# Kernel tuning notes

Hardware: AMD Instinct MI355X
Metric: run time of the kernel (lower is better)

## Reference

```python
import jax, jax.numpy as jnp
import numpy as np

N_HEADS = 4


def grid_sample_bilinear(img, grid):
    # img: (B, C, H, W); grid: (B, *S, 2) with (x, y) in [-1, 1]; torch bilinear, align_corners=True
    B, C, H, W = img.shape
    sp = grid.shape[1:-1]
    g = grid.reshape(B, -1, 2)
    x = (g[..., 0] + 1.0) * 0.5 * (W - 1)
    y = (g[..., 1] + 1.0) * 0.5 * (H - 1)
    x0 = jnp.floor(x)
    y0 = jnp.floor(y)
    wx = x - x0
    wy = y - y0
    x0i = jnp.clip(x0, 0, W - 1).astype(jnp.int32)
    x1i = jnp.clip(x0 + 1, 0, W - 1).astype(jnp.int32)
    y0i = jnp.clip(y0, 0, H - 1).astype(jnp.int32)
    y1i = jnp.clip(y0 + 1, 0, H - 1).astype(jnp.int32)
    flat = img.reshape(B, C, H * W)
    take = jax.vmap(lambda f, i: f[:, i])  # (C, HW), (N,) -> (C, N)
    out = (take(flat, y0i * W + x0i) * ((1 - wx) * (1 - wy))[:, None, :]
           + take(flat, y0i * W + x1i) * (wx * (1 - wy))[:, None, :]
           + take(flat, y1i * W + x0i) * ((1 - wx) * wy)[:, None, :]
           + take(flat, y1i * W + x1i) * (wx * wy)[:, None, :])
    return out.reshape((B, C) + sp)


def dw_conv_k4s4(x, w, b):
    # depthwise conv, kernel=4, stride=4, pad=0 (kernel == stride): non-overlapping patches
    B, C, H, W = x.shape
    xr = x.reshape(B, C, H // 4, 4, W // 4, 4)
    return jnp.einsum('bchpwq,cpq->bchw', xr, w) + b[None, :, None, None]


def ln_channels(x, g, b, eps=1e-5):
    # LayerNormProxy: LayerNorm over channel dim of NCHW
    mu = jnp.mean(x, axis=1, keepdims=True)
    var = jnp.var(x, axis=1, keepdims=True)
    return (x - mu) * jax.lax.rsqrt(var + eps) * g[None, :, None, None] + b[None, :, None, None]


def ref_points(Hk, Wk):
    ry = jnp.linspace(0.5, Hk - 0.5, Hk) / (Hk - 1.0) * 2.0 - 1.0
    rx = jnp.linspace(0.5, Wk - 0.5, Wk) / (Wk - 1.0) * 2.0 - 1.0
    return jnp.stack(jnp.meshgrid(ry, rx, indexing='ij'), axis=-1)  # (Hk, Wk, 2) as (y, x)


def q_grid(H, W):
    ry = jnp.arange(H, dtype=jnp.float32) / (H - 1.0) * 2.0 - 1.0
    rx = jnp.arange(W, dtype=jnp.float32) / (W - 1.0) * 2.0 - 1.0
    return jnp.stack(jnp.meshgrid(ry, rx, indexing='ij'), axis=-1).reshape(H * W, 2)


def dat_block(x, p):
    # DAttentionBaseline: n_groups=1, stride=ksize=4, offset_range_factor=-1, use_pe (learned rpe table)
    dw_w, dw_b, ln_g, ln_b, pw_w, wq, bq, wk, bk, wv, bv, wo, bo, rpe = p
    B, C, H, W = x.shape
    hc = C // N_HEADS
    scale = hc ** -0.5
    q = jnp.einsum('oc,bchw->bohw', wq, x) + bq[None, :, None, None]
    t = jax.nn.gelu(ln_channels(dw_conv_k4s4(q, dw_w, dw_b), ln_g, ln_b), approximate=False)
    off = jnp.einsum('oc,bchw->bohw', pw_w, t)  # (B, 2, Hk, Wk), channels = (dy, dx)
    Hk, Wk = off.shape[2], off.shape[3]
    ns = Hk * Wk
    pos = jnp.clip(off.transpose(0, 2, 3, 1) + ref_points(Hk, Wk)[None], -1.0, 1.0)  # (B,Hk,Wk,2) (y,x)
    xs = grid_sample_bilinear(x, pos[..., ::-1]).reshape(B, C, ns)  # kv == q input here
    k = jnp.einsum('oc,bcn->bon', wk, xs) + bk[None, :, None]
    v = jnp.einsum('oc,bcn->bon', wv, xs) + bv[None, :, None]
    qh = q.reshape(B, N_HEADS, hc, H * W)
    attn = jnp.einsum('bhcm,bhcn->bhmn', qh, k.reshape(B, N_HEADS, hc, ns)) * scale
    disp = (q_grid(H, W)[None, :, None, :] - pos.reshape(B, 1, ns, 2)) * 0.5  # (B, HW, ns, 2) (y,x)
    rpe_b = jnp.broadcast_to(rpe[None], (B,) + rpe.shape)
    attn = attn + grid_sample_bilinear(rpe_b, disp[..., ::-1])  # (B, heads, HW, ns)
    attn = jax.nn.softmax(attn, axis=-1)
    out = jnp.einsum('bhmn,bhcn->bhcm', attn, v.reshape(B, N_HEADS, hc, ns)).reshape(B, C, H, W)
    return jnp.einsum('oc,bchw->bohw', wo, out) + bo[None, :, None, None]


def _block_params(key, c, H, W):
    ks = jax.random.split(key, 7)
    return dict(
        off_dw_w=0.05 * jax.random.normal(ks[0], (c, 4, 4), dtype=jnp.float32),
        off_dw_b=jnp.zeros((c,), jnp.float32),
        ln_g=jnp.ones((c,), jnp.float32),
        ln_b=jnp.zeros((c,), jnp.float32),
        off_pw_w=0.02 * jax.random.normal(ks[1], (2, c), dtype=jnp.float32),
        wq=0.02 * jax.random.normal(ks[2], (c, c), dtype=jnp.float32),
        bq=jnp.zeros((c,), jnp.float32),
        wk=0.02 * jax.random.normal(ks[3], (c, c), dtype=jnp.float32),
        bk=jnp.zeros((c,), jnp.float32),
        wv=0.02 * jax.random.normal(ks[4], (c, c), dtype=jnp.float32),
        bv=jnp.zeros((c,), jnp.float32),
        wo=0.02 * jax.random.normal(ks[5], (c, c), dtype=jnp.float32),
        bo=jnp.zeros((c,), jnp.float32),
        rpe=0.01 * jax.random.normal(ks[6], (N_HEADS, 2 * H - 1, 2 * W - 1), dtype=jnp.float32),
    )


def setup_inputs() -> dict:
    key = jax.random.key(0)
    k0, k1, k2 = jax.random.split(key, 3)
    B, C, H, W = 8, 512, 64, 64
    inp = {'x0': jax.random.normal(k0, (B, C, H, W), dtype=jnp.float32)}
    for pre, k in (('sc_', k1), ('tr_', k2)):
        for n, v in _block_params(k, C // 2, H, W).items():
            inp[pre + n] = v
    return inp


def reference(x0,
              sc_off_dw_w, sc_off_dw_b, sc_ln_g, sc_ln_b, sc_off_pw_w, sc_wq, sc_bq, sc_wk, sc_bk,
              sc_wv, sc_bv, sc_wo, sc_bo, sc_rpe,
              tr_off_dw_w, tr_off_dw_b, tr_ln_g, tr_ln_b, tr_off_pw_w, tr_wq, tr_bq, tr_wk, tr_bk,
              tr_wv, tr_bv, tr_wo, tr_bo, tr_rpe):
    B, C, H, W = x0.shape
    qc1 = C // 2
    q = x0[:, :qc1]
    sc_p = (sc_off_dw_w, sc_off_dw_b, sc_ln_g, sc_ln_b, sc_off_pw_w, sc_wq, sc_bq, sc_wk, sc_bk,
            sc_wv, sc_bv, sc_wo, sc_bo, sc_rpe)
    tr_p = (tr_off_dw_w, tr_off_dw_b, tr_ln_g, tr_ln_b, tr_off_pw_w, tr_wq, tr_bq, tr_wk, tr_bk,
            tr_wv, tr_bv, tr_wo, tr_bo, tr_rpe)
    s = dat_block(q, sc_p)
    t = dat_block(q, tr_p)
    z = jnp.zeros((B, C - qc1, H, W), x0.dtype)
    scale_full = jnp.concatenate([z, s], axis=1)
    trans_full = jnp.concatenate([z, t], axis=1)
    res = x0 * jnp.exp(scale_full) + trans_full
    jac = jnp.sum(scale_full, axis=(1, 2, 3))[None, :]  # (n_vars=1, B)
    return res, jac
```

## Files before the change

kernel.cpp:

```cpp
#include <hip/hip_runtime.h>
#include <math.h>

typedef __bf16 bf16;
typedef __attribute__((ext_vector_type(8))) __bf16 bf16x8;
typedef __attribute__((ext_vector_type(4))) __bf16 bf16x4;
typedef __attribute__((ext_vector_type(4))) float floatx4;

#define MFMA16(a, b, c) __builtin_amdgcn_mfma_f32_16x16x32_bf16((a), (b), (c), 0, 0, 0)

__device__ __forceinline__ float bflo(unsigned d) {
    unsigned u = d << 16; float f; __builtin_memcpy(&f, &u, 4); return f;
}
__device__ __forceinline__ float bfhi(unsigned d) {
    unsigned u = d & 0xffff0000u; float f; __builtin_memcpy(&f, &u, 4); return f;
}

__device__ __forceinline__ void breduce1(float &a, float* lds, int t) {
    #pragma unroll
    for (int off = 32; off; off >>= 1) a += __shfl_xor(a, off, 64);
    __syncthreads();
    if ((t & 63) == 0) lds[t >> 6] = a;
    __syncthreads();
    a = lds[0] + lds[1] + lds[2] + lds[3];
}

__global__ __launch_bounds__(256) void init_kernel(const float* __restrict__ x0,
                                                   float* __restrict__ out) {
    int fi = blockIdx.x * 256 + threadIdx.x;
    int b = fi >> 18;
    int r = fi & 262143;
    const float4* src = (const float4*)x0;
    float4* dst = (float4*)out;
    dst[(size_t)b * 524288 + r] = src[(size_t)b * 524288 + r];
}

__global__ __launch_bounds__(256) void wconv(
    const float* __restrict__ w0, const float* __restrict__ w1,
    const float* __restrict__ w2, const float* __restrict__ w3,
    const float* __restrict__ w4, const float* __restrict__ w5,
    const float* __restrict__ w6, const float* __restrict__ w7,
    bf16* __restrict__ dst) {
    const int wi = blockIdx.y;
    const float* src = wi == 0 ? w0 : wi == 1 ? w1 : wi == 2 ? w2 : wi == 3 ? w3
                     : wi == 4 ? w4 : wi == 5 ? w5 : wi == 6 ? w6 : w7;
    const int i = blockIdx.x * 1024 + threadIdx.x * 4;
    const float4 v = *(const float4*)(src + i);
    bf16x4 h, l;
    #pragma unroll
    for (int j = 0; j < 4; j++) {
        const float f = ((const float*)&v)[j];
        const bf16 hb = (bf16)f;
        h[j] = hb;
        l[j] = (bf16)(f - (float)hb);
    }
    *(bf16x4*)(dst + (size_t)wi * 65536 + i) = h;
    *(bf16x4*)(dst + (size_t)(8 + wi) * 65536 + i) = l;
}

template <int MODE>
__global__ __launch_bounds__(256) void gemm_mfma(
    const void* __restrict__ Aptr, int ldA, long long bsA,
    const bf16* __restrict__ Whi, const bf16* __restrict__ Wlo,
    const float* __restrict__ bias,
    bf16* __restrict__ outb,
    float* outf,
    const float* __restrict__ x0full,
    float* __restrict__ jpart)
{
    constexpr bool ASPLIT = (MODE <= 2);
    __shared__ __align__(16) bf16 As_hi[128 * 40];
    __shared__ __align__(16) bf16 As_lo[ASPLIT ? 128 * 40 : 1];
    __shared__ __align__(16) bf16 Bs_hi[128 * 40];
    __shared__ __align__(16) bf16 Bs_lo[128 * 40];
    __shared__ float red[4];
    const int t = threadIdx.x;
    const int b = blockIdx.z;
    const int n0 = blockIdx.x * 128;
    const int o0 = blockIdx.y * 128;
    const int w = t >> 6, l = t & 63;
    const int wr = w & 1, wc = w >> 1;
    const int lr = l & 15, lq = l >> 4;

    floatx4 acc[4][4] = {};

    for (int kb = 0; kb < 8; kb++) {
        if (ASPLIT) {
            const float* Af = (const float*)Aptr + (size_t)b * bsA;
            #pragma unroll
            for (int s = 0; s < 4; s++) {
                const int kk = s * 8 + (t >> 5);
                const int n = (t & 31) * 4;
                const float4 v = *(const float4*)(Af + (size_t)(kb * 32 + kk) * ldA + n0 + n);
                #pragma unroll
                for (int j = 0; j < 4; j++) {
                    const float f = ((const float*)&v)[j];
                    const bf16 hb = (bf16)f;
                    As_hi[(n + j) * 40 + kk] = hb;
                    As_lo[(n + j) * 40 + kk] = (bf16)(f - (float)hb);
                }
            }
        } else {
            const bf16* Ab = (const bf16*)Aptr + (size_t)b * bsA;
            #pragma unroll
            for (int s = 0; s < 2; s++) {
                const int idx = t + 256 * s;
                const int row = idx >> 2, seg = idx & 3;
                *(bf16x8*)(As_hi + row * 40 + seg * 8) =
                    *(const bf16x8*)(Ab + (size_t)(n0 + row) * 256 + kb * 32 + seg * 8);
            }
        }
        #pragma unroll
        for (int s = 0; s < 2; s++) {
            const int idx = t + 256 * s;
            const int row = idx >> 2, seg = idx & 3;
            *(bf16x8*)(Bs_hi + row * 40 + seg * 8) =
                *(const bf16x8*)(Whi + (size_t)(o0 + row) * 256 + kb * 32 + seg * 8);
            *(bf16x8*)(Bs_lo + row * 40 + seg * 8) =
                *(const bf16x8*)(Wlo + (size_t)(o0 + row) * 256 + kb * 32 + seg * 8);
        }
        __syncthreads();
        bf16x8 ah[4], al[4], bh[4], bl[4];
        #pragma unroll
        for (int f = 0; f < 4; f++) {
            ah[f] = *(const bf16x8*)(As_hi + (wr * 64 + f * 16 + lr) * 40 + lq * 8);
            if (ASPLIT)
                al[f] = *(const bf16x8*)(As_lo + (wr * 64 + f * 16 + lr) * 40 + lq * 8);
            bh[f] = *(const bf16x8*)(Bs_hi + (wc * 64 + f * 16 + lr) * 40 + lq * 8);
            bl[f] = *(const bf16x8*)(Bs_lo + (wc * 64 + f * 16 + lr) * 40 + lq * 8);
        }
        #pragma unroll
        for (int i = 0; i < 4; i++)
            #pragma unroll
            for (int j = 0; j < 4; j++) {
                acc[i][j] = MFMA16(ah[i], bh[j], acc[i][j]);
                acc[i][j] = MFMA16(ah[i], bl[j], acc[i][j]);
                if (ASPLIT) acc[i][j] = MFMA16(al[i], bh[j], acc[i][j]);
            }
        __syncthreads();
    }

    float ssum = 0.0f;
    #pragma unroll
    for (int i = 0; i < 4; i++) {
        #pragma unroll
        for (int j = 0; j < 4; j++) {
            const int o_g = o0 + wc * 64 + j * 16 + lr;
            const int n_b = n0 + wr * 64 + i * 16 + lq * 4;
            const float bia = bias[o_g];
            floatx4 val = acc[i][j];
            val[0] += bia; val[1] += bia; val[2] += bia; val[3] += bia;
            if (MODE == 0) {
                *(floatx4*)(outf + (size_t)b * 2097152 + (size_t)o_g * 4096 + n_b) = val;
                #pragma unroll
                for (int r = 0; r < 4; r++)
                    outb[((size_t)b * 4096 + n_b + r) * 256 + o_g] = (bf16)val[r];
            } else {
                const size_t addr = (size_t)b * 2097152 + (size_t)(256 + o_g) * 4096 + n_b;
                if (MODE == 3) {
                    *(floatx4*)(outf + addr) = val;
                } else {
                    const floatx4 s4 = *(const floatx4*)(outf + addr);
                    const floatx4 x4 = *(const floatx4*)(x0full + addr);
                    floatx4 res;
                    #pragma unroll
                    for (int r = 0; r < 4; r++) res[r] = x4[r] * expf(s4[r]) + val[r];
                    *(floatx4*)(outf + addr) = res;
                    ssum += s4[0] + s4[1] + s4[2] + s4[3];
                }
            }
        }
    }
    if (MODE == 4) {
        breduce1(ssum, red, t);
        if (t == 0) jpart[b * 64 + blockIdx.y * 32 + blockIdx.x] = ssum;
    }
}

__global__ __launch_bounds__(256) void gemm_kv(
    const bf16* __restrict__ xs_hi, const bf16* __restrict__ xs_lo,
    const bf16* __restrict__ wkh, const bf16* __restrict__ wkl,
    const bf16* __restrict__ wvh, const bf16* __restrict__ wvl,
    const float* __restrict__ bk, const float* __restrict__ bv,
    bf16* __restrict__ kT, bf16* __restrict__ vbuf)
{
    __shared__ __align__(16) bf16 As_hi[128 * 40];
    __shared__ __align__(16) bf16 As_lo[128 * 40];
    __shared__ __align__(16) bf16 Bs_hi[128 * 40];
    __shared__ __align__(16) bf16 Bs_lo[128 * 40];
    const int t = threadIdx.x;
    const int b = blockIdx.z;
    const int n0 = blockIdx.x * 128;
    const int kv = blockIdx.y >> 1;
    const int o0 = (blockIdx.y & 1) * 128;
    const bf16* Whi = kv ? wvh : wkh;
    const bf16* Wlo = kv ? wvl : wkl;
    const float* bias = kv ? bv : bk;
    const int w = t >> 6, l = t & 63;
    const int wr = w & 1, wc = w >> 1;
    const int lr = l & 15, lq = l >> 4;

    floatx4 acc[4][4] = {};

    for (int kb = 0; kb < 8; kb++) {
        #pragma unroll
        for (int s = 0; s < 2; s++) {
            const int idx = t + 256 * s;
            const int row = idx >> 2, seg = idx & 3;
            const size_t asrc = ((size_t)b * 256 + n0 + row) * 256 + kb * 32 + seg * 8;
            *(bf16x8*)(As_hi + row * 40 + seg * 8) = *(const bf16x8*)(xs_hi + asrc);
            *(bf16x8*)(As_lo + row * 40 + seg * 8) = *(const bf16x8*)(xs_lo + asrc);
            *(bf16x8*)(Bs_hi + row * 40 + seg * 8) =
                *(const bf16x8*)(Whi + (size_t)(o0 + row) * 256 + kb * 32 + seg * 8);
            *(bf16x8*)(Bs_lo + row * 40 + seg * 8) =
                *(const bf16x8*)(Wlo + (size_t)(o0 + row) * 256 + kb * 32 + seg * 8);
        }
        __syncthreads();
        bf16x8 ah[4], al[4], bh[4], bl[4];
        #pragma unroll
        for (int f = 0; f < 4; f++) {
            ah[f] = *(const bf16x8*)(As_hi + (wr * 64 + f * 16 + lr) * 40 + lq * 8);
            al[f] = *(const bf16x8*)(As_lo + (wr * 64 + f * 16 + lr) * 40 + lq * 8);
            bh[f] = *(const bf16x8*)(Bs_hi + (wc * 64 + f * 16 + lr) * 40 + lq * 8);
            bl[f] = *(const bf16x8*)(Bs_lo + (wc * 64 + f * 16 + lr) * 40 + lq * 8);
        }
        #pragma unroll
        for (int i = 0; i < 4; i++)
            #pragma unroll
            for (int j = 0; j < 4; j++) {
                acc[i][j] = MFMA16(ah[i], bh[j], acc[i][j]);
                acc[i][j] = MFMA16(ah[i], bl[j], acc[i][j]);
                acc[i][j] = MFMA16(al[i], bh[j], acc[i][j]);
            }
        __syncthreads();
    }

    #pragma unroll
    for (int i = 0; i < 4; i++) {
        #pragma unroll
        for (int j = 0; j < 4; j++) {
            const int o_g = o0 + wc * 64 + j * 16 + lr;
            const int n_b = n0 + wr * 64 + i * 16 + lq * 4;
            const float bia = bias[o_g];
            floatx4 val = acc[i][j];
            val[0] += bia; val[1] += bia; val[2] += bia; val[3] += bia;
            if (kv == 0) {
                #pragma unroll
                for (int r = 0; r < 4; r++)
                    kT[((size_t)b * 256 + n_b + r) * 256 + o_g] = (bf16)val[r];
            } else {
                bf16x4 pv;
                pv[0] = (bf16)val[0]; pv[1] = (bf16)val[1];
                pv[2] = (bf16)val[2]; pv[3] = (bf16)val[3];
                *(bf16x4*)(vbuf + ((size_t)b * 256 + o_g) * 256 + n_b) = pv;
            }
        }
    }
}

__global__ __launch_bounds__(64) void jac_reduce(const float* __restrict__ jpart,
                                                 float* __restrict__ out) {
    const int b = blockIdx.x, t = threadIdx.x;
    float v = jpart[b * 64 + t];
    #pragma unroll
    for (int off = 32; off; off >>= 1) v += __shfl_xor(v, off, 64);
    if (t == 0) out[16777216 + b] = v;
}

__global__ __launch_bounds__(256) void offset_kernel(
    const float* __restrict__ q,
    const float* __restrict__ dw_w, const float* __restrict__ dw_b,
    const float* __restrict__ ln_g, const float* __restrict__ ln_b,
    const float* __restrict__ pw_w,
    float* __restrict__ pos)
{
    __shared__ float red[8];
    const int wk = blockIdx.x, hk = blockIdx.y, b = blockIdx.z;
    const int c = threadIdx.x;
    const float* qp = q + (size_t)b * 2097152 + (size_t)c * 4096 + (hk * 4) * 64 + wk * 4;
    float accv = dw_b[c];
    #pragma unroll
    for (int p = 0; p < 4; p++) {
        const float4 r = *(const float4*)(qp + p * 64);
        const float4 w = *(const float4*)(dw_w + c * 16 + p * 4);
        accv += r.x * w.x + r.y * w.y + r.z * w.z + r.w * w.w;
    }
    float a = accv, sq = accv * accv;
    #pragma unroll
    for (int off = 32; off; off >>= 1) {
        a += __shfl_xor(a, off, 64);
        sq += __shfl_xor(sq, off, 64);
    }
    __syncthreads();
    if ((c & 63) == 0) { red[c >> 6] = a; red[4 + (c >> 6)] = sq; }
    __syncthreads();
    a = red[0] + red[1] + red[2] + red[3];
    sq = red[4] + red[5] + red[6] + red[7];
    const float mu = a * (1.0f / 256.0f);
    const float var = sq * (1.0f / 256.0f) - mu * mu;
    float nrm = (accv - mu) * rsqrtf(var + 1e-5f) * ln_g[c] + ln_b[c];
    const float act = 0.5f * nrm * (1.0f + erff(nrm * 0.70710678118654752f));
    float v0 = pw_w[c] * act;
    float v1 = pw_w[256 + c] * act;
    #pragma unroll
    for (int off = 32; off; off >>= 1) {
        v0 += __shfl_xor(v0, off, 64);
        v1 += __shfl_xor(v1, off, 64);
    }
    __syncthreads();
    if ((c & 63) == 0) { red[c >> 6] = v0; red[4 + (c >> 6)] = v1; }
    __syncthreads();
    if (c == 0) {
        v0 = red[0] + red[1] + red[2] + red[3];
        v1 = red[4] + red[5] + red[6] + red[7];
        const float refy = (0.5f + hk) * (2.0f / 15.0f) - 1.0f;
        const float refx = (0.5f + wk) * (2.0f / 15.0f) - 1.0f;
        const float py = fminf(fmaxf(v0 + refy, -1.0f), 1.0f);
        const float px = fminf(fmaxf(v1 + refx, -1.0f), 1.0f);
        const int n = hk * 16 + wk;
        pos[(b * 256 + n) * 2] = py;
        pos[(b * 256 + n) * 2 + 1] = px;
    }
}

__global__ __launch_bounds__(256) void sample_kernel(
    const float* __restrict__ x0,
    const float* __restrict__ pos,
    bf16* __restrict__ xs_hi,
    bf16* __restrict__ xs_lo)
{
    const int c = threadIdx.x, n = blockIdx.x, b = blockIdx.y;
    const float py = pos[(b * 256 + n) * 2];
    const float px = pos[(b * 256 + n) * 2 + 1];
    const float x = (px + 1.0f) * 31.5f;
    const float y = (py + 1.0f) * 31.5f;
    const float xf = floorf(x), yf = floorf(y);
    const float wx = x - xf, wy = y - yf;
    const int xi0 = min(max((int)xf, 0), 63);
    const int xi1 = min(xi0 + 1, 63);
    const int yi0 = min(max((int)yf, 0), 63);
    const int yi1 = min(yi0 + 1, 63);
    const float* base = x0 + (size_t)b * 2097152 + (size_t)c * 4096;
    const float v00 = base[yi0 * 64 + xi0], v01 = base[yi0 * 64 + xi1];
    const float v10 = base[yi1 * 64 + xi0], v11 = base[yi1 * 64 + xi1];
    const float f =
        v00 * (1 - wx) * (1 - wy) + v01 * wx * (1 - wy) +
        v10 * (1 - wx) * wy + v11 * wx * wy;
    const bf16 hb = (bf16)f;
    const size_t addr = ((size_t)b * 256 + n) * 256 + c;
    xs_hi[addr] = hb;
    xs_lo[addr] = (bf16)(f - (float)hb);
}

__global__ __launch_bounds__(256, 4) void attn_mfma(
    const bf16* qbfT,
    const bf16* __restrict__ kT,
    const bf16* __restrict__ vb,
    const float* __restrict__ pos,
    const float* __restrict__ rpe,
    bf16* obfT)
{
    __shared__ __align__(16) bf16 pl[16896];
    __shared__ float wxs[256];
    const int t = threadIdx.x;
    const int w = t >> 6, l = t & 63;
    const int lr = l & 15, lq = l >> 4;
    const int m_base = blockIdx.x * 64 + w * 16;
    const int my = blockIdx.x;
    const int h = blockIdx.y, b = blockIdx.z;

    const float2 pp = *(const float2*)(pos + (b * 256 + t) * 2);
    const float yy = (float)my + 63.0f - 31.5f * pp.x;
    const float xo = 63.0f - 31.5f * pp.y;
    const float yfl = floorf(yy);
    const float wy_r = yy - yfl;
    const int y0 = min((int)yfl, 126);
    const int o0_r = y0 * 127;
    const int o1_r = min(y0 + 1, 126) * 127;
    const int xb_r = (int)floorf(xo);
    wxs[t] = xo - (float)xb_r;

    const float* rp = rpe + h * 16129;

    const bf16* qrow = qbfT + ((size_t)b * 4096 + m_base + lr) * 256 + h * 64;
    const bf16x8 qf0 = *(const bf16x8*)(qrow + lq * 8);
    const bf16x8 qf1 = *(const bf16x8*)(qrow + 32 + lq * 8);

    #pragma unroll 8
    for (int i = 0; i < 64; i++) {
        const int xb = __shfl(xb_r, i);
        const float wy = __shfl(wy_r, i);
        const int o0 = __shfl(o0_r, i);
        const int o1 = __shfl(o1_r, i);
        const int xj = min(xb + l, 126);
        const float v0 = rp[o0 + xj];
        const float v1 = rp[o1 + xj];
        pl[(w * 64 + i) * 66 + l] = (bf16)fmaf(wy, v1 - v0, v0);
    }
    {
        const int xe = min(xb_r + 64, 126);
        const float e0 = rp[o0_r + xe];
        const float e1 = rp[o1_r + xe];
        pl[t * 66 + 64] = (bf16)fmaf(wy_r, e1 - e0, e0);
    }
    __syncthreads();

    float mrun[4] = {-1e30f, -1e30f, -1e30f, -1e30f};
    float srun[4] = {0.0f, 0.0f, 0.0f, 0.0f};
    floatx4 oc[4] = {};
    bf16* plw = pl + w * 2112;

    #pragma unroll
    for (int c = 0; c < 2; c++) {
        floatx4 lg[8];
        #pragma unroll
        for (int nf = 0; nf < 8; nf++) {
            const bf16* krow = kT + ((size_t)b * 256 + c * 128 + nf * 16 + lr) * 256 + h * 64;
            const bf16x8 k0 = *(const bf16x8*)(krow + lq * 8);
            const bf16x8 k1 = *(const bf16x8*)(krow + 32 + lq * 8);
            floatx4 a = {};
            a = MFMA16(qf0, k0, a);
            a = MFMA16(qf1, k1, a);
            lg[nf] = a;
        }

        #pragma unroll
        for (int nf = 0; nf < 8; nf++) {
            const int n = c * 128 + nf * 16 + lr;
            const unsigned* rw = (const unsigned*)(pl + n * 66 + w * 16 + lq * 4);
            const unsigned d0 = rw[0], d1 = rw[1], d2 = rw[2];
            float rv[5];
            rv[0] = bflo(d0); rv[1] = bfhi(d0);
            rv[2] = bflo(d1); rv[3] = bfhi(d1);
            rv[4] = bflo(d2);
            const float wxv = wxs[n];
            #pragma unroll
            for (int r = 0; r < 4; r++)
                lg[nf][r] = lg[nf][r] * 0.125f + (rv[r] + wxv * (rv[r + 1] - rv[r]));
        }

        #pragma unroll
        for (int r = 0; r < 4; r++) {
            float m = lg[0][r];
            #pragma unroll
            for (int nf = 1; nf < 8; nf++) m = fmaxf(m, lg[nf][r]);
            #pragma unroll
            for (int off = 1; off < 16; off <<= 1) m = fmaxf(m, __shfl_xor(m, off, 64));
            const float mn = fmaxf(mrun[r], m);
            const float sc = __expf(mrun[r] - mn);
            mrun[r] = mn;
            float s = 0.0f;
            #pragma unroll
            for (int nf = 0; nf < 8; nf++) {
                const float e = __expf(lg[nf][r] - mn);
                lg[nf][r] = e;
                s += e;
            }
            #pragma unroll
            for (int off = 1; off < 16; off <<= 1) s += __shfl_xor(s, off, 64);
            srun[r] = srun[r] * sc + s;
            oc[0][r] *= sc; oc[1][r] *= sc; oc[2][r] *= sc; oc[3][r] *= sc;
        }

        if (c == 0) __syncthreads();

        #pragma unroll
        for (int nf = 0; nf < 8; nf++)
            #pragma unroll
            for (int r = 0; r < 4; r++)
                plw[(lq * 4 + r) * 132 + nf * 16 + lr] = (bf16)lg[nf][r];

        #pragma unroll
        for (int kf = 0; kf < 4; kf++) {
            const bf16x8 pa = *(const bf16x8*)(plw + lr * 132 + kf * 32 + lq * 8);
            #pragma unroll
            for (int j = 0; j < 4; j++) {
                const bf16x8 vf = *(const bf16x8*)(
                    vb + ((size_t)b * 256 + h * 64 + j * 16 + lr) * 256 + c * 128 + kf * 32 + lq * 8);
                oc[j] = MFMA16(pa, vf, oc[j]);
            }
        }
    }

    float inv[4];
    #pragma unroll
    for (int r = 0; r < 4; r++) inv[r] = 1.0f / srun[r];

    bf16* ot = plw;
    #pragma unroll
    for (int j = 0; j < 4; j++)
        #pragma unroll
        for (int r = 0; r < 4; r++)
            ot[(lq * 4 + r) * 72 + j * 16 + lr] = (bf16)(oc[j][r] * inv[r]);
    const int mrow = l >> 2, seg = l & 3;
    const bf16x8 ov0 = *(const bf16x8*)(ot + mrow * 72 + seg * 8);
    const bf16x8 ov1 = *(const bf16x8*)(ot + mrow * 72 + (4 + seg) * 8);
    bf16* orow = obfT + ((size_t)b * 4096 + m_base + mrow) * 256 + h * 64;
    *(bf16x8*)(orow + seg * 8) = ov0;
    *(bf16x8*)(orow + (4 + seg) * 8) = ov1;
}

extern "C" void kernel_launch(void* const* d_in, const int* in_sizes, int n_in,
                              void* d_out, int out_size, void* d_ws, size_t ws_size,
                              hipStream_t stream) {
    const float* x0 = (const float*)d_in[0];
    float* out = (float*)d_out;
    float* ws = (float*)d_ws;
    bf16* qbfT  = (bf16*)ws;
    bf16* xs_hi = (bf16*)(ws + 4194304);
    bf16* xs_lo = xs_hi + 524288;
    bf16* kTb   = (bf16*)(ws + 4718592);
    bf16* vbb   = (bf16*)(ws + 4980736);
    bf16* wbf   = (bf16*)(ws + 5242880);
    float* pos  = ws + 5767168;
    float* jpart= ws + 5771264;

    wconv<<<dim3(64, 8), 256, 0, stream>>>(
        (const float*)d_in[6], (const float*)d_in[8], (const float*)d_in[10],
        (const float*)d_in[12], (const float*)d_in[20], (const float*)d_in[22],
        (const float*)d_in[24], (const float*)d_in[26], wbf);

    for (int pass = 0; pass < 2; pass++) {
        const int pb = 1 + 14 * pass;
        const float* dw_w = (const float*)d_in[pb + 0];
        const float* dw_b = (const float*)d_in[pb + 1];
        const float* ln_g = (const float*)d_in[pb + 2];
        const float* ln_b = (const float*)d_in[pb + 3];
        const float* pw_w = (const float*)d_in[pb + 4];
        const float* bq   = (const float*)d_in[pb + 6];
        const float* bk   = (const float*)d_in[pb + 8];
        const float* bv   = (const float*)d_in[pb + 10];
        const float* bo   = (const float*)d_in[pb + 12];
        const float* rpe  = (const float*)d_in[pb + 13];
        const bf16* wq_h = wbf + (size_t)(pass * 4 + 0) * 65536;
        const bf16* wk_h = wbf + (size_t)(pass * 4 + 1) * 65536;
        const bf16* wv_h = wbf + (size_t)(pass * 4 + 2) * 65536;
        const bf16* wo_h = wbf + (size_t)(pass * 4 + 3) * 65536;
        const bf16* wq_l = wq_h + 8 * 65536;
        const bf16* wk_l = wk_h + 8 * 65536;
        const bf16* wv_l = wv_h + 8 * 65536;
        const bf16* wo_l = wo_h + 8 * 65536;

        gemm_mfma<0><<<dim3(32, 2, 8), 256, 0, stream>>>(
            x0, 4096, 2097152LL, wq_h, wq_l, bq, qbfT, out, nullptr, nullptr);
        offset_kernel<<<dim3(16, 16, 8), 256, 0, stream>>>(
            out, dw_w, dw_b, ln_g, ln_b, pw_w, pos);
        sample_kernel<<<dim3(256, 8), 256, 0, stream>>>(x0, pos, xs_hi, xs_lo);
        gemm_kv<<<dim3(2, 4, 8), 256, 0, stream>>>(
            xs_hi, xs_lo, wk_h, wk_l, wv_h, wv_l, bk, bv, kTb, vbb);
        attn_mfma<<<dim3(64, 4, 8), 256, 0, stream>>>(
            qbfT, kTb, vbb, pos, rpe, qbfT);
        if (pass == 0)
            gemm_mfma<3><<<dim3(32, 2, 8), 256, 0, stream>>>(
                qbfT, 256, 1048576LL, wo_h, wo_l, bo, nullptr, out, nullptr, nullptr);
        else
            gemm_mfma<4><<<dim3(32, 2, 8), 256, 0, stream>>>(
                qbfT, 256, 1048576LL, wo_h, wo_l, bo, nullptr, out, x0, jpart);
    }
    init_kernel<<<8192, 256, 0, stream>>>(x0, out);
    jac_reduce<<<8, 64, 0, stream>>>(jpart, out);
}
```

Baseline: 624.7 us.

## Read padded RPE table directly in attention instead of staging bias in LDS

Adds a kernel that copies the relative-position table into a row-padded (160-wide) fp32 buffer that reuses the freed xs workspace. The attention kernel then reads bilinear bias samples straight from global/L2 with vector loads, no longer prebuilding a per-block bf16 bias tile in shared memory. This shrinks LDS use so the launch bound rises to 6 blocks per CU, and it drops one barrier. In exchange it adds a kernel launch and more scattered global loads inside the inner loop. Bias precision also rises from bf16 to fp32.

```diff
diff --git a/kernel.cpp b/kernel.cpp
--- a/kernel.cpp
+++ b/kernel.cpp
@@ -7,13 +7,6 @@
 typedef __attribute__((ext_vector_type(4))) float floatx4;
 
 #define MFMA16(a, b, c) __builtin_amdgcn_mfma_f32_16x16x32_bf16((a), (b), (c), 0, 0, 0)
-
-__device__ __forceinline__ float bflo(unsigned d) {
-    unsigned u = d << 16; float f; __builtin_memcpy(&f, &u, 4); return f;
-}
-__device__ __forceinline__ float bfhi(unsigned d) {
-    unsigned u = d & 0xffff0000u; float f; __builtin_memcpy(&f, &u, 4); return f;
-}
 
 __device__ __forceinline__ void breduce1(float &a, float* lds, int t) {
     #pragma unroll
@@ -55,6 +48,15 @@
     }
     *(bf16x4*)(dst + (size_t)wi * 65536 + i) = h;
     *(bf16x4*)(dst + (size_t)(8 + wi) * 65536 + i) = l;
+}
+
+__global__ __launch_bounds__(256) void rpe_pad(const float* __restrict__ rpe,
+                                               float* __restrict__ dst) {
+    const int x = threadIdx.x;
+    const int y = blockIdx.x;
+    const int h = blockIdx.y;
+    if (x < 160)
+        dst[(h * 127 + y) * 160 + x] = rpe[h * 16129 + y * 127 + min(x, 126)];
 }
 
 template <int MODE>
@@ -351,16 +353,17 @@
     xs_lo[addr] = (bf16)(f - (float)hb);
 }
 
-__global__ __launch_bounds__(256, 4) void attn_mfma(
+__global__ __launch_bounds__(256, 6) void attn_mfma(
     const bf16* qbfT,
     const bf16* __restrict__ kT,
     const bf16* __restrict__ vb,
     const float* __restrict__ pos,
-    const float* __restrict__ rpe,
+    const float* __restrict__ rpp,
     bf16* obfT)
 {
-    __shared__ __align__(16) bf16 pl[16896];
-    __shared__ float wxs[256];
+    __shared__ __align__(16) bf16 pl[8448];
+    __shared__ unsigned b01s[256];
+    __shared__ float2 wyxs[256];
     const int t = threadIdx.x;
     const int w = t >> 6, l = t & 63;
     const int lr = l & 15, lq = l >> 4;
@@ -372,36 +375,20 @@
     const float yy = (float)my + 63.0f - 31.5f * pp.x;
     const float xo = 63.0f - 31.5f * pp.y;
     const float yfl = floorf(yy);
-    const float wy_r = yy - yfl;
+    const float xfl = floorf(xo);
     const int y0 = min((int)yfl, 126);
-    const int o0_r = y0 * 127;
-    const int o1_r = min(y0 + 1, 126) * 127;
-    const int xb_r = (int)floorf(xo);
-    wxs[t] = xo - (float)xb_r;
-
-    const float* rp = rpe + h * 16129;
+    const int y1 = min(y0 + 1, 126);
+    const int xb = (int)xfl;
+    b01s[t] = (unsigned)(y0 * 160 + xb) | ((unsigned)(y1 * 160 + xb) << 16);
+    wyxs[t] = make_float2(yy - yfl, xo - xfl);
+
+    const float* rp = rpp + h * 20320;
+    const int mxw = w * 16 + lq * 4;
 
     const bf16* qrow = qbfT + ((size_t)b * 4096 + m_base + lr) * 256 + h * 64;
     const bf16x8 qf0 = *(const bf16x8*)(qrow + lq * 8);
     const bf16x8 qf1 = *(const bf16x8*)(qrow + 32 + lq * 8);
 
-    #pragma unroll 8
-    for (int i = 0; i < 64; i++) {
-        const int xb = __shfl(xb_r, i);
-        const float wy = __shfl(wy_r, i);
-        const int o0 = __shfl(o0_r, i);
-        const int o1 = __shfl(o1_r, i);
-        const int xj = min(xb + l, 126);
-        const float v0 = rp[o0 + xj];
-        const float v1 = rp[o1 + xj];
-        pl[(w * 64 + i) * 66 + l] = (bf16)fmaf(wy, v1 - v0, v0);
-    }
-    {
-        const int xe = min(xb_r + 64, 126);
-        const float e0 = rp[o0_r + xe];
-        const float e1 = rp[o1_r + xe];
-        pl[t * 66 + 64] = (bf16)fmaf(wy_r, e1 - e0, e0);
-    }
     __syncthreads();
 
     float mrun[4] = {-1e30f, -1e30f, -1e30f, -1e30f};
@@ -426,16 +413,25 @@
         #pragma unroll
         for (int nf = 0; nf < 8; nf++) {
             const int n = c * 128 + nf * 16 + lr;
-            const unsigned* rw = (const unsigned*)(pl + n * 66 + w * 16 + lq * 4);
-            const unsigned d0 = rw[0], d1 = rw[1], d2 = rw[2];
+            const unsigned bb = b01s[n];
+            const float2 wv = wyxs[n];
+            const float* p0 = rp + (bb & 0xffffu) + mxw;
+            const float* p1 = rp + (bb >> 16) + mxw;
+            floatx4 a0, a1;
+            __builtin_memcpy(&a0, p0, 16);
+            __builtin_memcpy(&a1, p1, 16);
+            const float e0 = p0[4], e1 = p1[4];
             float rv[5];
-            rv[0] = bflo(d0); rv[1] = bfhi(d0);
-            rv[2] = bflo(d1); rv[3] = bfhi(d1);
-            rv[4] = bflo(d2);
-            const float wxv = wxs[n];
-            #pragma unroll
-            for (int r = 0; r < 4; r++)
-                lg[nf][r] = lg[nf][r] * 0.125f + (rv[r] + wxv * (rv[r + 1] - rv[r]));
+            rv[0] = fmaf(wv.x, a1[0] - a0[0], a0[0]);
+            rv[1] = fmaf(wv.x, a1[1] - a0[1], a0[1]);
+            rv[2] = fmaf(wv.x, a1[2] - a0[2], a0[2]);
+            rv[3] = fmaf(wv.x, a1[3] - a0[3], a0[3]);
+            rv[4] = fmaf(wv.x, e1 - e0, e0);
+            #pragma unroll
+            for (int r = 0; r < 4; r++) {
+                const float bias = fmaf(wv.y, rv[r + 1] - rv[r], rv[r]);
+                lg[nf][r] = fmaf(lg[nf][r], 0.125f, bias);
+            }
         }
 
         #pragma unroll
@@ -460,8 +456,6 @@
             srun[r] = srun[r] * sc + s;
             oc[0][r] *= sc; oc[1][r] *= sc; oc[2][r] *= sc; oc[3][r] *= sc;
         }
-
-        if (c == 0) __syncthreads();
 
         #pragma unroll
         for (int nf = 0; nf < 8; nf++)
@@ -508,6 +502,7 @@
     bf16* qbfT  = (bf16*)ws;
     bf16* xs_hi = (bf16*)(ws + 4194304);
     bf16* xs_lo = xs_hi + 524288;
+    float* rpad = ws + 4194304;
     bf16* kTb   = (bf16*)(ws + 4718592);
     bf16* vbb   = (bf16*)(ws + 4980736);
     bf16* wbf   = (bf16*)(ws + 5242880);
@@ -547,8 +542,9 @@
         sample_kernel<<<dim3(256, 8), 256, 0, stream>>>(x0, pos, xs_hi, xs_lo);
         gemm_kv<<<dim3(2, 4, 8), 256, 0, stream>>>(
             xs_hi, xs_lo, wk_h, wk_l, wv_h, wv_l, bk, bv, kTb, vbb);
+        rpe_pad<<<dim3(127, 4), 256, 0, stream>>>(rpe, rpad);
         attn_mfma<<<dim3(64, 4, 8), 256, 0, stream>>>(
-            qbfT, kTb, vbb, pos, rpe, qbfT);
+            qbfT, kTb, vbb, pos, rpad, qbfT);
         if (pass == 0)
             gemm_mfma<3><<<dim3(32, 2, 8), 256, 0, stream>>>(
                 qbfT, 256, 1048576LL, wo_h, wo_l, bo, nullptr, out, nullptr, nullptr);
```

Result: slower. 683.8 us (+9.5%).

## Halve attention LDS by building RPE bias per key chunk, raise occupancy

Applied to the files above, without the earlier changes.

The interpolated relative-position bias table is no longer built for all 256 keys up front. It is now built per 128-key chunk inside the chunk loop, so the shared buffer shrinks by half and is reused for both the bias and the probability tile. Launch bounds go from 4 to 8 blocks per CU to exploit the smaller LDS footprint, and the shuffled per-key offsets are packed into fewer registers. This costs an extra barrier per chunk and tighter register budgets, which may cause spills.

```diff
diff --git a/kernel.cpp b/kernel.cpp
--- a/kernel.cpp
+++ b/kernel.cpp
@@ -351,7 +351,7 @@
     xs_lo[addr] = (bf16)(f - (float)hb);
 }
 
-__global__ __launch_bounds__(256, 4) void attn_mfma(
+__global__ __launch_bounds__(256, 8) void attn_mfma(
     const bf16* qbfT,
     const bf16* __restrict__ kT,
     const bf16* __restrict__ vb,
@@ -359,7 +359,7 @@
     const float* __restrict__ rpe,
     bf16* obfT)
 {
-    __shared__ __align__(16) bf16 pl[16896];
+    __shared__ __align__(16) bf16 buf[8448];
     __shared__ float wxs[256];
     const int t = threadIdx.x;
     const int w = t >> 6, l = t & 63;
@@ -368,16 +368,19 @@
     const int my = blockIdx.x;
     const int h = blockIdx.y, b = blockIdx.z;
 
-    const float2 pp = *(const float2*)(pos + (b * 256 + t) * 2);
+    const int n_own = w * 32 + (l & 31) + ((l >> 5) << 7);
+    const float2 pp = *(const float2*)(pos + (b * 256 + n_own) * 2);
     const float yy = (float)my + 63.0f - 31.5f * pp.x;
     const float xo = 63.0f - 31.5f * pp.y;
     const float yfl = floorf(yy);
+    const float xfl = floorf(xo);
+    const int y0 = min((int)yfl, 126);
+    const int y1 = min(y0 + 1, 126);
+    const int xb = (int)xfl;
     const float wy_r = yy - yfl;
-    const int y0 = min((int)yfl, 126);
-    const int o0_r = y0 * 127;
-    const int o1_r = min(y0 + 1, 126) * 127;
-    const int xb_r = (int)floorf(xo);
-    wxs[t] = xo - (float)xb_r;
+    wxs[n_own] = xo - xfl;
+    const int u0 = (y0 * 127 + xb) | ((126 - xb) << 16);
+    const int u1 = y1 * 127 + xb;
 
     const float* rp = rpe + h * 16129;
 
@@ -385,57 +388,56 @@
     const bf16x8 qf0 = *(const bf16x8*)(qrow + lq * 8);
     const bf16x8 qf1 = *(const bf16x8*)(qrow + 32 + lq * 8);
 
-    #pragma unroll 8
-    for (int i = 0; i < 64; i++) {
-        const int xb = __shfl(xb_r, i);
-        const float wy = __shfl(wy_r, i);
-        const int o0 = __shfl(o0_r, i);
-        const int o1 = __shfl(o1_r, i);
-        const int xj = min(xb + l, 126);
-        const float v0 = rp[o0 + xj];
-        const float v1 = rp[o1 + xj];
-        pl[(w * 64 + i) * 66 + l] = (bf16)fmaf(wy, v1 - v0, v0);
-    }
-    {
-        const int xe = min(xb_r + 64, 126);
-        const float e0 = rp[o0_r + xe];
-        const float e1 = rp[o1_r + xe];
-        pl[t * 66 + 64] = (bf16)fmaf(wy_r, e1 - e0, e0);
-    }
-    __syncthreads();
-
     float mrun[4] = {-1e30f, -1e30f, -1e30f, -1e30f};
     float srun[4] = {0.0f, 0.0f, 0.0f, 0.0f};
     floatx4 oc[4] = {};
-    bf16* plw = pl + w * 2112;
+    bf16* plw = buf + w * 2112;
 
     #pragma unroll
     for (int c = 0; c < 2; c++) {
+        #pragma unroll 8
+        for (int i = 0; i < 32; i++) {
+            const int src = (c << 5) + i;
+            const int a0 = __shfl(u0, src);
+            const int a1 = __shfl(u1, src);
+            const float wyi = __shfl(wy_r, src);
+            const int xoff = min(l, a0 >> 16);
+            const float v0 = rp[(a0 & 0xffff) + xoff];
+            const float v1 = rp[a1 + xoff];
+            buf[(w * 32 + i) * 66 + l] = (bf16)fmaf(wyi, v1 - v0, v0);
+        }
+        if ((l >> 5) == c) {
+            const int xoff = min(64, u0 >> 16);
+            const float v0 = rp[(u0 & 0xffff) + xoff];
+            const float v1 = rp[u1 + xoff];
+            buf[(w * 32 + (l & 31)) * 66 + 64] = (bf16)fmaf(wy_r, v1 - v0, v0);
+        }
+
         floatx4 lg[8];
         #pragma unroll
         for (int nf = 0; nf < 8; nf++) {
             const bf16* krow = kT + ((size_t)b * 256 + c * 128 + nf * 16 + lr) * 256 + h * 64;
-            const bf16x8 k0 = *(const bf16x8*)(krow + lq * 8);
-            const bf16x8 k1 = *(const bf16x8*)(krow + 32 + lq * 8);
             floatx4 a = {};
-            a = MFMA16(qf0, k0, a);
-            a = MFMA16(qf1, k1, a);
+            a = MFMA16(qf0, *(const bf16x8*)(krow + lq * 8), a);
+            a = MFMA16(qf1, *(const bf16x8*)(krow + 32 + lq * 8), a);
             lg[nf] = a;
         }
 
+        __syncthreads();
+
         #pragma unroll
         for (int nf = 0; nf < 8; nf++) {
-            const int n = c * 128 + nf * 16 + lr;
-            const unsigned* rw = (const unsigned*)(pl + n * 66 + w * 16 + lq * 4);
+            const int rbuf = nf * 16 + lr;
+            const unsigned* rw = (const unsigned*)(buf + rbuf * 66 + w * 16 + lq * 4);
             const unsigned d0 = rw[0], d1 = rw[1], d2 = rw[2];
             float rv[5];
             rv[0] = bflo(d0); rv[1] = bfhi(d0);
             rv[2] = bflo(d1); rv[3] = bfhi(d1);
             rv[4] = bflo(d2);
-            const float wxv = wxs[n];
+            const float wxv = wxs[c * 128 + rbuf];
             #pragma unroll
             for (int r = 0; r < 4; r++)
-                lg[nf][r] = lg[nf][r] * 0.125f + (rv[r] + wxv * (rv[r + 1] - rv[r]));
+                lg[nf][r] = fmaf(lg[nf][r], 0.125f, fmaf(wxv, rv[r + 1] - rv[r], rv[r]));
         }
 
         #pragma unroll
@@ -461,7 +463,7 @@
             oc[0][r] *= sc; oc[1][r] *= sc; oc[2][r] *= sc; oc[3][r] *= sc;
         }
 
-        if (c == 0) __syncthreads();
+        __syncthreads();
 
         #pragma unroll
         for (int nf = 0; nf < 8; nf++)
```

New measurement: 643.8 us. +3.1%, slower.
